# Optimization experiments

Measured on AMD Instinct MI355X. Metric: run time of the kernel, lower is better.

## Reference

```python
import jax, jax.numpy as jnp
import numpy as np

L, B, T, D, H, F, V = 4, 2, 1024, 1024, 16, 4096, 32000
DH = D // H
POWER = 4
EPS = 1e-6


def _anorm(x, gain):
    # y = g * x / (mean(|x|) + eps)  (L1 'diamond' norm)
    return gain * (x / (jnp.mean(jnp.abs(x), axis=-1, keepdims=True) + EPS))


def _rational_softmax(x):
    s = x / (jnp.abs(x) + 1.0)          # squash to (-1, 1)
    p = ((s + 1.0) * 0.5) ** POWER      # shift to (0,1), sharpen
    return p / (jnp.sum(p, axis=-1, keepdims=True) + EPS)


def setup_inputs() -> dict:
    key = jax.random.key(0)
    ks = jax.random.split(key, 12)
    w = 0.02  # weight scale for stability
    return {
        "idx": jax.random.randint(ks[0], (B, T), 0, V),
        "tok_emb": jax.random.normal(ks[1], (V, D), jnp.float32) * w,
        "pos_emb": jax.random.normal(ks[2], (T, D), jnp.float32) * w,
        "Wq": jax.random.normal(ks[3], (L, D, D), jnp.float32) * w,
        "bq": jnp.zeros((L, D), jnp.float32),
        "Wk": jax.random.normal(ks[4], (L, D, D), jnp.float32) * w,
        "bk": jnp.zeros((L, D), jnp.float32),
        "Wv": jax.random.normal(ks[5], (L, D, D), jnp.float32) * w,
        "bv": jnp.zeros((L, D), jnp.float32),
        "Wo": jax.random.normal(ks[6], (L, D, D), jnp.float32) * w,
        "bo": jnp.zeros((L, D), jnp.float32),
        "score_gain": jnp.full((L,), 4.0, jnp.float32),
        "norm1_gain": jnp.ones((L, D), jnp.float32),
        "norm2_gain": jnp.ones((L, D), jnp.float32),
        "W1": jax.random.normal(ks[7], (L, D, F), jnp.float32) * w,
        "b1": jnp.zeros((L, F), jnp.float32),
        "W2": jax.random.normal(ks[8], (L, F, D), jnp.float32) * w,
        "b2": jnp.zeros((L, D), jnp.float32),
        "final_gain": jnp.ones((D,), jnp.float32),
        "Wlm": jax.random.normal(ks[9], (D, V), jnp.float32) * w,
        "blm": jnp.zeros((V,), jnp.float32),
    }


def _forward(idx, tok_emb, pos_emb, Wq, bq, Wk, bk, Wv, bv, Wo, bo,
             score_gain, norm1_gain, norm2_gain, W1, b1, W2, b2,
             final_gain, Wlm, blm):
    Bx, Tx = idx.shape
    x = tok_emb[idx] + pos_emb[:Tx]                 # [B,T,D]
    mask = jnp.triu(jnp.ones((Tx, Tx), bool), 1)    # causal mask (True = masked)
    for l in range(L):
        # --- algebraic attention ---
        h = _anorm(x, norm1_gain[l])
        q = (h @ Wq[l] + bq[l]).reshape(Bx, Tx, H, DH).transpose(0, 2, 1, 3)
        k = (h @ Wk[l] + bk[l]).reshape(Bx, Tx, H, DH).transpose(0, 2, 1, 3)
        v = (h @ Wv[l] + bv[l]).reshape(Bx, Tx, H, DH).transpose(0, 2, 1, 3)
        scores = jnp.einsum('bhqd,bhkd->bhqk', q, k)
        scores = scores - jnp.mean(scores, axis=-1, keepdims=True)
        mad = jnp.mean(jnp.abs(scores), axis=-1, keepdims=True) + EPS
        scores = (scores / mad) * score_gain[l]
        scores = jnp.where(mask, -1000.0, scores)
        attn = _rational_softmax(scores)
        o = jnp.einsum('bhqk,bhkd->bhqd', attn, v)
        o = o.transpose(0, 2, 1, 3).reshape(Bx, Tx, D)
        x = x + (o @ Wo[l] + bo[l])
        # --- FFN with algebraic ReLU ---
        h = _anorm(x, norm2_gain[l])
        h = jnp.maximum(h @ W1[l] + b1[l], 0.0)
        x = x + (h @ W2[l] + b2[l])
    x = _anorm(x, final_gain)
    return x @ Wlm + blm                            # [B,T,V] logits


def reference(idx, tok_emb, pos_emb, Wq, bq, Wk, bk, Wv, bv, Wo, bo,
              score_gain, norm1_gain, norm2_gain, W1, b1, W2, b2,
              final_gain, Wlm, blm):
    return _forward(idx, tok_emb, pos_emb, Wq, bq, Wk, bk, Wv, bv, Wo, bo,
                    score_gain, norm1_gain, norm2_gain, W1, b1, W2, b2,
                    final_gain, Wlm, blm)
```

## Files before the change

### kernel.cpp

```cpp
#include <hip/hip_runtime.h>

typedef unsigned short u16;
typedef __bf16 bf16x8 __attribute__((ext_vector_type(8)));
typedef float f32x4 __attribute__((ext_vector_type(4)));
typedef unsigned int u32;

#define EPSF 1e-6f

__device__ __forceinline__ u16 f2bf(float f) {
  union { float f; unsigned u; } un; un.f = f;
  unsigned r = un.u + 0x7FFFu + ((un.u >> 16) & 1u);
  return (u16)(r >> 16);
}

__device__ __forceinline__ float block_sum(float v) {
  #pragma unroll
  for (int off = 32; off > 0; off >>= 1) v += __shfl_xor(v, off, 64);
  __shared__ float ws[4];
  const int w = threadIdx.x >> 6;
  __syncthreads();
  if ((threadIdx.x & 63) == 0) ws[w] = v;
  __syncthreads();
  return ws[0] + ws[1] + ws[2] + ws[3];
}

__device__ __forceinline__ void lds_cp16(const void* g, void* l) {
  __builtin_amdgcn_global_load_lds(
      (__attribute__((address_space(1))) void*)g,
      (__attribute__((address_space(3))) void*)l, 16, 0, 0);
}

__global__ __launch_bounds__(256) void embed_norm(
    const int* __restrict__ idx, const float* __restrict__ tok,
    const float* __restrict__ pos, const float* __restrict__ gain,
    float* __restrict__ x, u16* __restrict__ h) {
  const int row = blockIdx.x;
  const int tpos = row & 1023;
  const int token = idx[row];
  const int d = threadIdx.x * 4;
  const float4 a = *(const float4*)(tok + (long)token * 1024 + d);
  const float4 b = *(const float4*)(pos + (long)tpos * 1024 + d);
  float4 o; o.x = a.x + b.x; o.y = a.y + b.y; o.z = a.z + b.z; o.w = a.w + b.w;
  *(float4*)(x + (long)row * 1024 + d) = o;
  float s = fabsf(o.x) + fabsf(o.y) + fabsf(o.z) + fabsf(o.w);
  s = block_sum(s);
  const float scale = 1.0f / (s * (1.0f / 1024.0f) + EPSF);
  const float4 g = *(const float4*)(gain + d);
  ushort4 ov;
  ov.x = f2bf(o.x * g.x * scale);
  ov.y = f2bf(o.y * g.y * scale);
  ov.z = f2bf(o.z * g.z * scale);
  ov.w = f2bf(o.w * g.w * scale);
  *(ushort4*)(h + (long)row * 1024 + d) = ov;
}

__global__ __launch_bounds__(256) void anorm_kernel(
    const float* __restrict__ x, const float* __restrict__ gain,
    u16* __restrict__ h) {
  const int row = blockIdx.x;
  const int tid = threadIdx.x;
  const float4 v = *(const float4*)(x + (long)row * 1024 + tid * 4);
  float s = fabsf(v.x) + fabsf(v.y) + fabsf(v.z) + fabsf(v.w);
  s = block_sum(s);
  const float scale = 1.0f / (s * (1.0f / 1024.0f) + EPSF);
  const float4 g = *(const float4*)(gain + tid * 4);
  ushort4 o;
  o.x = f2bf(v.x * g.x * scale);
  o.y = f2bf(v.y * g.y * scale);
  o.z = f2bf(v.z * g.z * scale);
  o.w = f2bf(v.w * g.w * scale);
  *(ushort4*)(h + (long)row * 1024 + tid * 4) = o;
}

__global__ __launch_bounds__(512, 4) void attn_v4(
    const u16* __restrict__ qkv, const u16* __restrict__ v_t,
    u16* __restrict__ obuf, const float* __restrict__ score_gain, int l) {
  __shared__ float red1[2][4][16], red2[2][4][16], red3[2][4][16];
  __shared__ float Ured[2][4][16][68];
  __shared__ u16 Pl[8][640];
  const int qt = blockIdx.x, h = blockIdx.y, b = blockIdx.z;
  const int tid = threadIdx.x, w = tid >> 6, l64 = tid & 63;
  const int lq = l64 & 15, kgrp = l64 >> 4;
  const int wq = w >> 2, tq = w & 3;
  const int qglob = qt * 32 + wq * 16 + lq;
  const int qmax  = qt * 32 + wq * 16 + 15;
  const int tbase = tq * 256;
  const u16* Qg = qkv + (size_t)b * (1024 * 3072) + h * 64;
  const u16* Kg = Qg + 1024;
  const u16* Vt = v_t + (size_t)(b * 16 + h) * (64 * 1024);
  char* Pw = (char*)&Pl[w][0];

  bf16x8 qB0, qB1;
  {
    const u16* qp = Qg + (size_t)qglob * 3072 + (kgrp << 3);
    qB0 = *(const bf16x8*)qp;
    qB1 = *(const bf16x8*)(qp + 32);
  }

  f32x4 s[16];
  {
    const u16* Kl = Kg + (size_t)(tbase + lq) * 3072 + (kgrp << 3);
    #pragma unroll
    for (int tile = 0; tile < 16; tile++) {
      const u16* kp = Kl + (size_t)tile * (16 * 3072);
      const bf16x8 k0 = *(const bf16x8*)kp;
      const bf16x8 k1 = *(const bf16x8*)(kp + 32);
      f32x4 d = {0.f, 0.f, 0.f, 0.f};
      d = __builtin_amdgcn_mfma_f32_16x16x32_bf16(k0, qB0, d, 0, 0, 0);
      d = __builtin_amdgcn_mfma_f32_16x16x32_bf16(k1, qB1, d, 0, 0, 0);
      s[tile] = d;
    }
  }

  float ssum = 0.f;
  #pragma unroll
  for (int tile = 0; tile < 16; tile++)
    ssum += (s[tile][0] + s[tile][1]) + (s[tile][2] + s[tile][3]);
  ssum += __shfl_xor(ssum, 16, 64);
  ssum += __shfl_xor(ssum, 32, 64);
  if (l64 < 16) red1[wq][tq][l64] = ssum;
  __syncthreads();
  const float mean = (red1[wq][0][lq] + red1[wq][1][lq] +
                      red1[wq][2][lq] + red1[wq][3][lq]) * (1.0f / 1024.0f);

  float asum = 0.f;
  #pragma unroll
  for (int tile = 0; tile < 16; tile++)
    asum += fabsf(s[tile][0] - mean) + fabsf(s[tile][1] - mean) +
            fabsf(s[tile][2] - mean) + fabsf(s[tile][3] - mean);
  asum += __shfl_xor(asum, 16, 64);
  asum += __shfl_xor(asum, 32, 64);
  if (l64 < 16) red2[wq][tq][l64] = asum;
  __syncthreads();
  const float mad = (red2[wq][0][lq] + red2[wq][1][lq] +
                     red2[wq][2][lq] + red2[wq][3][lq]) * (1.0f / 1024.0f) + EPSF;
  const float gs = score_gain[l] / mad;

  float psum = 0.f;
  #pragma unroll
  for (int tile = 0; tile < 16; tile++) {
    #pragma unroll
    for (int j = 0; j < 4; j++) {
      const int t = tbase + tile * 16 + (kgrp << 2) + j;
      float sv = (s[tile][j] - mean) * gs;
      if (t > qglob) sv = -1000.0f;
      const float rr = sv / (fabsf(sv) + 1.0f);
      const float a1 = (rr + 1.0f) * 0.5f;
      const float a2 = a1 * a1;
      s[tile][j] = a2 * a2;
      psum += s[tile][j];
    }
  }

  f32x4 U[4] = {};
  #pragma unroll
  for (int c = 0; c < 8; c++) {
    const int t0 = tbase + c * 32;
    if (t0 <= qmax) {
      #pragma unroll
      for (int half = 0; half < 2; half++) {
        #pragma unroll
        for (int pr = 0; pr < 2; pr++) {
          const u32 pk = (u32)f2bf(s[2 * c + half][pr * 2]) |
                         ((u32)f2bf(s[2 * c + half][pr * 2 + 1]) << 16);
          *(u32*)(Pw + lq * 80 + half * 32 + (kgrp << 3) + (pr << 2)) = pk;
        }
      }
      asm volatile("s_waitcnt lgkmcnt(0)" ::: "memory");
      __builtin_amdgcn_sched_barrier(0);
      const bf16x8 pB = *(const bf16x8*)(Pw + lq * 80 + (kgrp << 4));
      #pragma unroll
      for (int dt = 0; dt < 4; dt++) {
        const bf16x8 vA = *(const bf16x8*)(Vt + (size_t)((dt << 4) + lq) * 1024 +
                                           t0 + (kgrp << 3));
        U[dt] = __builtin_amdgcn_mfma_f32_16x16x32_bf16(vA, pB, U[dt], 0, 0, 0);
      }
    }
  }

  psum += __shfl_xor(psum, 16, 64);
  psum += __shfl_xor(psum, 32, 64);
  if (l64 < 16) red3[wq][tq][l64] = psum;
  #pragma unroll
  for (int dt = 0; dt < 4; dt++)
    *(float4*)&Ured[wq][tq][lq][(dt << 4) + (kgrp << 2)] = *(const float4*)&U[dt];
  __syncthreads();

  {
    const int qq = tid >> 4, dhseg = (tid & 15) << 2;
    const int fwq = qq >> 4, flq = qq & 15;
    const float fps = red3[fwq][0][flq] + red3[fwq][1][flq] +
                      red3[fwq][2][flq] + red3[fwq][3][flq];
    const float oinv = 1.0f / (fps + EPSF);
    float4 u0 = *(const float4*)&Ured[fwq][0][flq][dhseg];
    const float4 u1 = *(const float4*)&Ured[fwq][1][flq][dhseg];
    const float4 u2 = *(const float4*)&Ured[fwq][2][flq][dhseg];
    const float4 u3 = *(const float4*)&Ured[fwq][3][flq][dhseg];
    u0.x = (u0.x + u1.x + u2.x + u3.x) * oinv;
    u0.y = (u0.y + u1.y + u2.y + u3.y) * oinv;
    u0.z = (u0.z + u1.z + u2.z + u3.z) * oinv;
    u0.w = (u0.w + u1.w + u2.w + u3.w) * oinv;
    ushort4 o;
    o.x = f2bf(u0.x); o.y = f2bf(u0.y); o.z = f2bf(u0.z); o.w = f2bf(u0.w);
    u16* dst = obuf + ((size_t)((b << 10) + qt * 32 + qq) << 10) + (h << 6) + dhseg;
    *(ushort4*)dst = o;
  }
}

__global__ void wconv_all(
    const float* __restrict__ Wq, const float* __restrict__ Wk,
    const float* __restrict__ Wv, const float* __restrict__ Wo,
    const float* __restrict__ W1, const float* __restrict__ W2,
    const float* __restrict__ Wlm,
    u16* __restrict__ wqkv_t, u16* __restrict__ wo_t,
    u16* __restrict__ w1_t, u16* __restrict__ w2_t, u16* __restrict__ wlm_t) {
  __shared__ float tile[64][65];
  const int bid = blockIdx.x;
  const float* src; u16* dst; int R, C, c0, r0;
  if (bid < 4096) {
    const int l = bid >> 10, m = (bid >> 8) & 3, t = bid & 255;
    if (m == 0)      src = Wq + (size_t)l * 1048576;
    else if (m == 1) src = Wk + (size_t)l * 1048576;
    else if (m == 2) src = Wv + (size_t)l * 1048576;
    else             src = Wo + (size_t)l * 1048576;
    dst = (m < 3) ? wqkv_t + ((size_t)l * 3072 + m * 1024) * 1024
                  : wo_t + (size_t)l * 1048576;
    R = 1024; C = 1024; c0 = (t & 15) << 6; r0 = (t >> 4) << 6;
  } else if (bid < 8192) {
    const int i = bid - 4096, l = i >> 10, t = i & 1023;
    src = W1 + (size_t)l * 4194304; dst = w1_t + (size_t)l * 4194304;
    R = 1024; C = 4096; c0 = (t & 63) << 6; r0 = (t >> 6) << 6;
  } else if (bid < 12288) {
    const int i = bid - 8192, l = i >> 10, t = i & 1023;
    src = W2 + (size_t)l * 4194304; dst = w2_t + (size_t)l * 4194304;
    R = 4096; C = 1024; c0 = (t & 15) << 6; r0 = (t >> 4) << 6;
  } else {
    const int i = bid - 12288;
    src = Wlm; dst = wlm_t;
    R = 1024; C = 32000; c0 = (i % 500) << 6; r0 = (i / 500) << 6;
  }
  const int tx = threadIdx.x, ty = threadIdx.y;
  const int cg = (tx & 15) << 2;
  const int rg = tx >> 4;
  #pragma unroll
  for (int i = 0; i < 4; i++) {
    const int row = i * 16 + ty * 4 + rg;
    const float4 v = *(const float4*)&src[(long)(r0 + row) * C + c0 + cg];
    tile[row][cg] = v.x; tile[row][cg + 1] = v.y;
    tile[row][cg + 2] = v.z; tile[row][cg + 3] = v.w;
  }
  __syncthreads();
  #pragma unroll
  for (int i = 0; i < 4; i++) {
    const int c = i * 16 + ty * 4 + rg;
    ushort4 o;
    o.x = f2bf(tile[cg][c]);     o.y = f2bf(tile[cg + 1][c]);
    o.z = f2bf(tile[cg + 2][c]); o.w = f2bf(tile[cg + 3][c]);
    *(ushort4*)&dst[(long)(c0 + c) * R + r0 + cg] = o;
  }
}

__global__ __launch_bounds__(256) void bias_concat(
    const float* __restrict__ bq, const float* __restrict__ bk,
    const float* __restrict__ bv, float* __restrict__ out) {
  const int i = blockIdx.x * 256 + threadIdx.x;
  const int l = i / 3072, j = i % 3072;
  float v;
  if (j < 1024)      v = bq[l * 1024 + j];
  else if (j < 2048) v = bk[l * 1024 + j - 1024];
  else               v = bv[l * 1024 + j - 2048];
  out[i] = v;
}

__global__ __launch_bounds__(256) void ffn2_reduce_norm(
    const float* __restrict__ part, const float* __restrict__ b2,
    float* __restrict__ x, const float* __restrict__ gain,
    u16* __restrict__ h) {
  const int row = blockIdx.x, c = threadIdx.x * 4;
  const float4 p0 = *(const float4*)(part + (size_t)row * 1024 + c);
  const float4 p1 = *(const float4*)(part + (size_t)(row + 2048) * 1024 + c);
  const float4 p2 = *(const float4*)(part + (size_t)(row + 4096) * 1024 + c);
  const float4 p3 = *(const float4*)(part + (size_t)(row + 6144) * 1024 + c);
  const float4 bb = *(const float4*)(b2 + c);
  float4 xv = *(float4*)(x + (size_t)row * 1024 + c);
  xv.x += (p0.x + p1.x) + (p2.x + p3.x) + bb.x;
  xv.y += (p0.y + p1.y) + (p2.y + p3.y) + bb.y;
  xv.z += (p0.z + p1.z) + (p2.z + p3.z) + bb.z;
  xv.w += (p0.w + p1.w) + (p2.w + p3.w) + bb.w;
  *(float4*)(x + (size_t)row * 1024 + c) = xv;
  float s = fabsf(xv.x) + fabsf(xv.y) + fabsf(xv.z) + fabsf(xv.w);
  s = block_sum(s);
  const float scale = 1.0f / (s * (1.0f / 1024.0f) + EPSF);
  const float4 g = *(const float4*)(gain + c);
  ushort4 o;
  o.x = f2bf(xv.x * g.x * scale);
  o.y = f2bf(xv.y * g.y * scale);
  o.z = f2bf(xv.z * g.z * scale);
  o.w = f2bf(xv.w * g.w * scale);
  *(ushort4*)(h + (size_t)row * 1024 + c) = o;
}

template <bool OUT_BF16, bool BIAS, bool RELU, bool RESID>
__global__ __launch_bounds__(512) void gemm256_kernel(
    const u16* __restrict__ A, long lda,
    const u16* __restrict__ Bt, long ldb,
    void* __restrict__ Cv, long ldc,
    const float* __restrict__ bias, const float* __restrict__ resid,
    int M, int N, int K, int nTM) {
  __shared__ u16 lds[65536];
  const int nwg = gridDim.x;
  const int qx = nwg >> 3, rx = nwg & 7;
  const int xcd = blockIdx.x & 7, seq = blockIdx.x >> 3;
  const int wg = (xcd < rx ? xcd * (qx + 1) : rx * (qx + 1) + (xcd - rx) * qx) + seq;
  const int tm = wg % nTM, tn = wg / nTM;
  const int rowA0 = tm * 256, rowB0 = tn * 256;

  const int t = threadIdx.x, w = t >> 6, l = t & 63;
  const int lrow = l & 15, kgrp = l >> 4;
  const int wr = w >> 2, wc = w & 3;

  const int srow = t >> 2;
  const int scol = ((t & 3) ^ ((t >> 3) & 3)) * 8;
  const u16* Asrc = A + (long)(rowA0 + srow) * lda + scol;
  const u16* Bsrc = Bt + (long)(rowB0 + srow) * ldb + scol;
  char* ldsB = (char*)lds;
  const int wbase = w * 1024;

  const int fswz = (kgrp ^ ((lrow >> 1) & 3)) * 8;
  const int aoff = (wr * 128 + lrow) * 32 + fswz;
  const int boff = 8192 + (wc * 64 + lrow) * 32 + fswz;

  f32x4 acc[8][4] = {};
  const int NT = K >> 5;

  #pragma unroll
  for (int pt = 0; pt < 3; pt++) {
    const int k0 = pt << 5;
    const int bb = pt * 32768;
    lds_cp16(Asrc + k0,                    ldsB + bb + wbase);
    lds_cp16(Asrc + (long)128 * lda + k0,  ldsB + bb + 8192 + wbase);
    lds_cp16(Bsrc + k0,                    ldsB + bb + 16384 + wbase);
    lds_cp16(Bsrc + (long)128 * ldb + k0,  ldsB + bb + 24576 + wbase);
  }

  for (int tt = 0; tt < NT; tt++) {
    const int rem = NT - 1 - tt;
    if (rem >= 2)      asm volatile("s_waitcnt vmcnt(8)" ::: "memory");
    else if (rem == 1) asm volatile("s_waitcnt vmcnt(4)" ::: "memory");
    else               asm volatile("s_waitcnt vmcnt(0)" ::: "memory");
    __builtin_amdgcn_sched_barrier(0);
    __builtin_amdgcn_s_barrier();

    const u16* buf = lds + (tt & 3) * 16384;
    const int stage = tt + 3 < NT;
    const int k0n = (tt + 3) << 5;
    const int bbn = ((tt + 3) & 3) * 32768;

    bf16x8 aF[4], bF[4];
    #pragma unroll
    for (int m = 0; m < 4; m++) aF[m] = *(const bf16x8*)(buf + aoff + m * 512);
    #pragma unroll
    for (int n = 0; n < 4; n++) bF[n] = *(const bf16x8*)(buf + boff + n * 512);
    if (stage) {
      lds_cp16(Asrc + k0n,                   ldsB + bbn + wbase);
      lds_cp16(Asrc + (long)128 * lda + k0n, ldsB + bbn + 8192 + wbase);
    }
    asm volatile("s_waitcnt lgkmcnt(0)" ::: "memory");
    __builtin_amdgcn_sched_barrier(0);
    __builtin_amdgcn_s_setprio(1);
    #pragma unroll
    for (int m = 0; m < 4; m++)
      #pragma unroll
      for (int n = 0; n < 4; n++)
        acc[m][n] = __builtin_amdgcn_mfma_f32_16x16x32_bf16(aF[m], bF[n], acc[m][n], 0, 0, 0);
    __builtin_amdgcn_s_setprio(0);

    #pragma unroll
    for (int m = 0; m < 4; m++) aF[m] = *(const bf16x8*)(buf + aoff + (m + 4) * 512);
    if (stage) {
      lds_cp16(Bsrc + k0n,                   ldsB + bbn + 16384 + wbase);
      lds_cp16(Bsrc + (long)128 * ldb + k0n, ldsB + bbn + 24576 + wbase);
    }
    asm volatile("s_waitcnt lgkmcnt(0)" ::: "memory");
    __builtin_amdgcn_sched_barrier(0);
    __builtin_amdgcn_s_setprio(1);
    #pragma unroll
    for (int m = 0; m < 4; m++)
      #pragma unroll
      for (int n = 0; n < 4; n++)
        acc[m + 4][n] = __builtin_amdgcn_mfma_f32_16x16x32_bf16(aF[m], bF[n], acc[m + 4][n], 0, 0, 0);
    __builtin_amdgcn_s_setprio(0);
  }

  float bvv[4];
  #pragma unroll
  for (int n = 0; n < 4; n++)
    bvv[n] = BIAS ? bias[rowB0 + wc * 64 + n * 16 + lrow] : 0.0f;
  #pragma unroll
  for (int m = 0; m < 8; m++) {
    const int row = rowA0 + wr * 128 + m * 16 + kgrp * 4;
    #pragma unroll
    for (int n = 0; n < 4; n++) {
      const int col = rowB0 + wc * 64 + n * 16 + lrow;
      #pragma unroll
      for (int j = 0; j < 4; j++) {
        float v = acc[m][n][j] + bvv[n];
        if (RELU) v = fmaxf(v, 0.0f);
        const long off = (long)(row + j) * ldc + col;
        if (RESID) v += resid[off];
        if (OUT_BF16) ((u16*)Cv)[off] = f2bf(v);
        else          ((float*)Cv)[off] = v;
      }
    }
  }
}

template <bool OUT_BF16, bool BIAS, bool RELU, bool RESID, bool VTOUT>
__global__ __launch_bounds__(256) void gemm128p(
    const u16* __restrict__ A, long lda, long sA,
    const u16* __restrict__ Bt, long ldb, long sB,
    void* __restrict__ Cv, long ldc, long sC,
    const float* __restrict__ bias, const float* __restrict__ resid,
    u16* __restrict__ vtout,
    int M, int N, int K, int nTM) {
  __shared__ u16 lds[32768];
  const int nwg = gridDim.x;
  const int qx = nwg >> 3, rx = nwg & 7;
  const int xcd = blockIdx.x & 7, seq = blockIdx.x >> 3;
  const int wg = (xcd < rx ? xcd * (qx + 1) : rx * (qx + 1) + (xcd - rx) * qx) + seq;
  const int tm = wg % nTM, tn = wg / nTM;
  const int batch = blockIdx.y;
  A  += (long)batch * sA;
  Bt += (long)batch * sB;
  const int rowA0 = tm * 128, rowB0 = tn * 128;
  const int t = threadIdx.x, w = t >> 6, l = t & 63;
  const int lrow = l & 15, kgrp = l >> 4;
  const int wr = (w >> 1) << 6, wc = (w & 1) << 6;

  const int srow = t >> 2;
  const int scol = ((t & 3) ^ ((t >> 3) & 3)) * 8;
  const u16* Asrc = A + (long)(rowA0 + srow) * lda + scol;
  const u16* Bsrc = Bt + (long)(rowB0 + srow) * ldb + scol;
  char* ldsB = (char*)lds;
  const int wbase = w * 1024;

  const int swz8 = (kgrp ^ ((lrow >> 1) & 3)) * 8;
  const int aoff = (wr + lrow) * 32 + swz8;
  const int boff = 4096 + (wc + lrow) * 32 + swz8;

  f32x4 acc[4][4] = {};
  const int NT = K >> 5;

  #pragma unroll
  for (int pt = 0; pt < 3; pt++) {
    const int k0 = pt << 5;
    const int bb = pt * 16384;
    lds_cp16(Asrc + k0,                   ldsB + bb + wbase);
    lds_cp16(Asrc + (long)64 * lda + k0,  ldsB + bb + 4096 + wbase);
    lds_cp16(Bsrc + k0,                   ldsB + bb + 8192 + wbase);
    lds_cp16(Bsrc + (long)64 * ldb + k0,  ldsB + bb + 12288 + wbase);
  }

  for (int tt = 0; tt < NT; tt++) {
    const int rem = NT - 1 - tt;
    if (rem >= 2)      asm volatile("s_waitcnt vmcnt(8)" ::: "memory");
    else if (rem == 1) asm volatile("s_waitcnt vmcnt(4)" ::: "memory");
    else               asm volatile("s_waitcnt vmcnt(0)" ::: "memory");
    __builtin_amdgcn_sched_barrier(0);
    __builtin_amdgcn_s_barrier();

    const u16* buf = lds + (tt & 3) * 8192;
    const int stage = tt + 3 < NT;
    const int k0n = (tt + 3) << 5;
    const int bbn = ((tt + 3) & 3) * 16384;

    bf16x8 aF[4], bF[4];
    #pragma unroll
    for (int m = 0; m < 4; m++) aF[m] = *(const bf16x8*)(buf + aoff + m * 512);
    #pragma unroll
    for (int n = 0; n < 4; n++) bF[n] = *(const bf16x8*)(buf + boff + n * 512);
    if (stage) {
      lds_cp16(Asrc + k0n,                  ldsB + bbn + wbase);
      lds_cp16(Asrc + (long)64 * lda + k0n, ldsB + bbn + 4096 + wbase);
      lds_cp16(Bsrc + k0n,                  ldsB + bbn + 8192 + wbase);
      lds_cp16(Bsrc + (long)64 * ldb + k0n, ldsB + bbn + 12288 + wbase);
    }
    asm volatile("s_waitcnt lgkmcnt(0)" ::: "memory");
    __builtin_amdgcn_sched_barrier(0);
    __builtin_amdgcn_s_setprio(1);
    #pragma unroll
    for (int m = 0; m < 4; m++)
      #pragma unroll
      for (int n = 0; n < 4; n++)
        acc[m][n] = __builtin_amdgcn_mfma_f32_16x16x32_bf16(aF[m], bF[n], acc[m][n], 0, 0, 0);
    __builtin_amdgcn_s_setprio(0);
  }

  if (VTOUT && rowB0 >= 2048) {
    __syncthreads();
    #pragma unroll
    for (int m = 0; m < 4; m++) {
      #pragma unroll
      for (int n = 0; n < 4; n++) {
        const int c = wc + n * 16 + lrow;
        const int r = wr + m * 16 + (kgrp << 2);
        ushort4 pk;
        float v0 = acc[m][n][0], v1 = acc[m][n][1], v2 = acc[m][n][2], v3 = acc[m][n][3];
        if (BIAS) {
          const float bv = bias[rowB0 + c];
          v0 += bv; v1 += bv; v2 += bv; v3 += bv;
        }
        pk.x = f2bf(v0); pk.y = f2bf(v1); pk.z = f2bf(v2); pk.w = f2bf(v3);
        *(ushort4*)&lds[c * 136 + r] = pk;
      }
    }
    __syncthreads();
    {
      const int c = t >> 1, half = t & 1;
      const int dh = c & 63;
      const int h = ((rowB0 - 2048) >> 6) + (c >> 6);
      const int bb2 = rowA0 >> 10, t0 = rowA0 & 1023;
      u16* dst = vtout + (((size_t)(bb2 * 16 + h)) << 16) + ((size_t)dh << 10) +
                 t0 + half * 64;
      #pragma unroll
      for (int k = 0; k < 8; k++)
        *(bf16x8*)(dst + k * 8) = *(const bf16x8*)&lds[c * 136 + half * 64 + k * 8];
    }
  } else {
    const long coff = (long)batch * sC;
    #pragma unroll
    for (int m = 0; m < 4; m++) {
      #pragma unroll
      for (int n = 0; n < 4; n++) {
        const int col = rowB0 + wc + n * 16 + lrow;
        #pragma unroll
        for (int j = 0; j < 4; j++) {
          const int row = rowA0 + wr + m * 16 + (kgrp << 2) + j;
          float v = acc[m][n][j];
          if (BIAS) v += bias[col];
          if (RELU) v = fmaxf(v, 0.0f);
          const long off = coff + (long)row * ldc + col;
          if (RESID) v += resid[off];
          if (OUT_BF16) ((u16*)Cv)[off] = f2bf(v);
          else          ((float*)Cv)[off] = v;
        }
      }
    }
  }
}

extern "C" void kernel_launch(void* const* d_in, const int* in_sizes, int n_in,
                              void* d_out, int out_size, void* d_ws, size_t ws_size,
                              hipStream_t stream) {
  constexpr int Lc = 4, Tc = 1024, Dc = 1024, Hc = 16, Fc = 4096, DHc = 64;
  const int M = 2 * Tc;

  const int*   idxp       = (const int*)  d_in[0];
  const float* tok_emb    = (const float*)d_in[1];
  const float* pos_emb    = (const float*)d_in[2];
  const float* Wq         = (const float*)d_in[3];
  const float* bq         = (const float*)d_in[4];
  const float* Wk         = (const float*)d_in[5];
  const float* bk         = (const float*)d_in[6];
  const float* Wv         = (const float*)d_in[7];
  const float* bv         = (const float*)d_in[8];
  const float* Wo         = (const float*)d_in[9];
  const float* bo         = (const float*)d_in[10];
  const float* score_gain = (const float*)d_in[11];
  const float* norm1_gain = (const float*)d_in[12];
  const float* norm2_gain = (const float*)d_in[13];
  const float* W1         = (const float*)d_in[14];
  const float* b1         = (const float*)d_in[15];
  const float* W2         = (const float*)d_in[16];
  const float* b2         = (const float*)d_in[17];
  const float* final_gain = (const float*)d_in[18];
  const float* Wlm        = (const float*)d_in[19];
  const float* blm        = (const float*)d_in[20];

  char* p = (char*)d_ws;
  auto alloc = [&](size_t n) { char* r = p; p += (n + 255) & ~(size_t)255; return r; };
  u16*  wqkv_t = (u16*) alloc((size_t)Lc * 3072 * 1024 * 2);
  u16*  wo_t   = (u16*) alloc((size_t)Lc * 1024 * 1024 * 2);
  u16*  w1_t   = (u16*) alloc((size_t)Lc * 4096 * 1024 * 2);
  u16*  w2_t   = (u16*) alloc((size_t)Lc * 1024 * 4096 * 2);
  u16*  wlm_t  = (u16*) alloc((size_t)32000 * 1024 * 2);
  float* bqkv  = (float*)alloc((size_t)Lc * 3072 * 4);
  float* x     = (float*)alloc((size_t)M * 1024 * 4);
  u16*  hbuf   = (u16*) alloc((size_t)M * 1024 * 2);
  u16*  qkv    = (u16*) alloc((size_t)M * 3072 * 2);
  u16*  v_t    = (u16*) alloc((size_t)2 * Hc * DHc * Tc * 2);
  u16*  obuf   = (u16*) alloc((size_t)M * 1024 * 2);
  u16*  ffh    = (u16*) alloc((size_t)M * 4096 * 2);
  float* fpart = (float*)alloc((size_t)4 * M * 1024 * 4);

  wconv_all<<<20288, dim3(64, 4), 0, stream>>>(Wq, Wk, Wv, Wo, W1, W2, Wlm,
                                               wqkv_t, wo_t, w1_t, w2_t, wlm_t);
  bias_concat<<<48, 256, 0, stream>>>(bq, bk, bv, bqkv);
  embed_norm<<<M, 256, 0, stream>>>(idxp, tok_emb, pos_emb, norm1_gain, x, hbuf);

  for (int l = 0; l < Lc; l++) {
    gemm128p<true, true, false, false, true><<<dim3(16 * 24, 1), 256, 0, stream>>>(
        hbuf, 1024, 0, wqkv_t + (size_t)l * 3072 * 1024, 1024, 0,
        qkv, 3072, 0, bqkv + (size_t)l * 3072, nullptr, v_t, M, 3072, 1024, 16);

    attn_v4<<<dim3(32, 16, 2), 512, 0, stream>>>(qkv, v_t, obuf, score_gain, l);

    gemm128p<false, true, false, true, false><<<dim3(16 * 8, 1), 256, 0, stream>>>(
        obuf, 1024, 0, wo_t + (size_t)l * 1024 * 1024, 1024, 0,
        x, 1024, 0, bo + (size_t)l * 1024, x, nullptr, M, 1024, 1024, 16);
    anorm_kernel<<<M, 256, 0, stream>>>(x, norm2_gain + (size_t)l * Dc, hbuf);
    gemm128p<true, true, true, false, false><<<dim3(16 * 32, 1), 256, 0, stream>>>(
        hbuf, 1024, 0, w1_t + (size_t)l * Fc * Dc, 1024, 0,
        ffh, 4096, 0, b1 + (size_t)l * Fc, nullptr, nullptr, M, 4096, 1024, 16);
    gemm128p<false, false, false, false, false><<<dim3(128, 4), 256, 0, stream>>>(
        ffh, 4096, 1024, w2_t + (size_t)l * Dc * Fc, 4096, 1024,
        fpart, 1024, (long)M * 1024, nullptr, nullptr, nullptr, M, 1024, 1024, 16);
    const float* gnext = (l < Lc - 1) ? (norm1_gain + (size_t)(l + 1) * Dc) : final_gain;
    ffn2_reduce_norm<<<M, 256, 0, stream>>>(fpart, b2 + (size_t)l * Dc, x, gnext, hbuf);
  }

  gemm256_kernel<false, true, false, false><<<dim3(1000), 512, 0, stream>>>(
      hbuf, 1024, wlm_t, 1024,
      d_out, 32000, blm, nullptr, M, 32000, 1024, 8);
}
```

Before: 990.9 us.

## Interleave attention key tiles across waves and split-K the output projection

```diff
diff --git a/kernel.cpp b/kernel.cpp
--- a/kernel.cpp
+++ b/kernel.cpp
@@ -54,25 +54,7 @@
   *(ushort4*)(h + (long)row * 1024 + d) = ov;
 }
 
-__global__ __launch_bounds__(256) void anorm_kernel(
-    const float* __restrict__ x, const float* __restrict__ gain,
-    u16* __restrict__ h) {
-  const int row = blockIdx.x;
-  const int tid = threadIdx.x;
-  const float4 v = *(const float4*)(x + (long)row * 1024 + tid * 4);
-  float s = fabsf(v.x) + fabsf(v.y) + fabsf(v.z) + fabsf(v.w);
-  s = block_sum(s);
-  const float scale = 1.0f / (s * (1.0f / 1024.0f) + EPSF);
-  const float4 g = *(const float4*)(gain + tid * 4);
-  ushort4 o;
-  o.x = f2bf(v.x * g.x * scale);
-  o.y = f2bf(v.y * g.y * scale);
-  o.z = f2bf(v.z * g.z * scale);
-  o.w = f2bf(v.w * g.w * scale);
-  *(ushort4*)(h + (long)row * 1024 + tid * 4) = o;
-}
-
-__global__ __launch_bounds__(512, 4) void attn_v4(
+__global__ __launch_bounds__(512, 4) void attn_v5(
     const u16* __restrict__ qkv, const u16* __restrict__ v_t,
     u16* __restrict__ obuf, const float* __restrict__ score_gain, int l) {
   __shared__ float red1[2][4][16], red2[2][4][16], red3[2][4][16];
@@ -84,7 +66,6 @@
   const int wq = w >> 2, tq = w & 3;
   const int qglob = qt * 32 + wq * 16 + lq;
   const int qmax  = qt * 32 + wq * 16 + 15;
-  const int tbase = tq * 256;
   const u16* Qg = qkv + (size_t)b * (1024 * 3072) + h * 64;
   const u16* Kg = Qg + 1024;
   const u16* Vt = v_t + (size_t)(b * 16 + h) * (64 * 1024);
@@ -99,23 +80,24 @@
 
   f32x4 s[16];
   {
-    const u16* Kl = Kg + (size_t)(tbase + lq) * 3072 + (kgrp << 3);
-    #pragma unroll
-    for (int tile = 0; tile < 16; tile++) {
-      const u16* kp = Kl + (size_t)tile * (16 * 3072);
+    const u16* Ktq = Kg + (size_t)(tq * 32 + lq) * 3072 + (kgrp << 3);
+    #pragma unroll
+    for (int tl = 0; tl < 16; tl++) {
+      const int cst = ((tl >> 1) << 7) + ((tl & 1) << 4);
+      const u16* kp = Ktq + (size_t)cst * 3072;
       const bf16x8 k0 = *(const bf16x8*)kp;
       const bf16x8 k1 = *(const bf16x8*)(kp + 32);
       f32x4 d = {0.f, 0.f, 0.f, 0.f};
       d = __builtin_amdgcn_mfma_f32_16x16x32_bf16(k0, qB0, d, 0, 0, 0);
       d = __builtin_amdgcn_mfma_f32_16x16x32_bf16(k1, qB1, d, 0, 0, 0);
-      s[tile] = d;
+      s[tl] = d;
     }
   }
 
   float ssum = 0.f;
   #pragma unroll
-  for (int tile = 0; tile < 16; tile++)
-    ssum += (s[tile][0] + s[tile][1]) + (s[tile][2] + s[tile][3]);
+  for (int tl = 0; tl < 16; tl++)
+    ssum += (s[tl][0] + s[tl][1]) + (s[tl][2] + s[tl][3]);
   ssum += __shfl_xor(ssum, 16, 64);
   ssum += __shfl_xor(ssum, 32, 64);
   if (l64 < 16) red1[wq][tq][l64] = ssum;
@@ -125,9 +107,9 @@
 
   float asum = 0.f;
   #pragma unroll
-  for (int tile = 0; tile < 16; tile++)
-    asum += fabsf(s[tile][0] - mean) + fabsf(s[tile][1] - mean) +
-            fabsf(s[tile][2] - mean) + fabsf(s[tile][3] - mean);
+  for (int tl = 0; tl < 16; tl++)
+    asum += fabsf(s[tl][0] - mean) + fabsf(s[tl][1] - mean) +
+            fabsf(s[tl][2] - mean) + fabsf(s[tl][3] - mean);
   asum += __shfl_xor(asum, 16, 64);
   asum += __shfl_xor(asum, 32, 64);
   if (l64 < 16) red2[wq][tq][l64] = asum;
@@ -138,42 +120,47 @@
 
   float psum = 0.f;
   #pragma unroll
-  for (int tile = 0; tile < 16; tile++) {
+  for (int tl = 0; tl < 16; tl++) {
+    const int tbase = tq * 32 + ((tl >> 1) << 7) + ((tl & 1) << 4);
     #pragma unroll
     for (int j = 0; j < 4; j++) {
-      const int t = tbase + tile * 16 + (kgrp << 2) + j;
-      float sv = (s[tile][j] - mean) * gs;
+      const int t = tbase + (kgrp << 2) + j;
+      float sv = (s[tl][j] - mean) * gs;
       if (t > qglob) sv = -1000.0f;
       const float rr = sv / (fabsf(sv) + 1.0f);
       const float a1 = (rr + 1.0f) * 0.5f;
       const float a2 = a1 * a1;
-      s[tile][j] = a2 * a2;
-      psum += s[tile][j];
+      s[tl][j] = a2 * a2;
+      psum += s[tl][j];
     }
   }
 
   f32x4 U[4] = {};
-  #pragma unroll
-  for (int c = 0; c < 8; c++) {
-    const int t0 = tbase + c * 32;
-    if (t0 <= qmax) {
-      #pragma unroll
-      for (int half = 0; half < 2; half++) {
+  {
+    const u16* Vtq = Vt + (size_t)lq * 1024 + tq * 32 + (kgrp << 3);
+    #pragma unroll
+    for (int cc = 0; cc < 8; cc++) {
+      const int t0 = tq * 32 + (cc << 7);
+      if (t0 <= qmax) {
+        bf16x8 vA[4];
         #pragma unroll
-        for (int pr = 0; pr < 2; pr++) {
-          const u32 pk = (u32)f2bf(s[2 * c + half][pr * 2]) |
-                         ((u32)f2bf(s[2 * c + half][pr * 2 + 1]) << 16);
-          *(u32*)(Pw + lq * 80 + half * 32 + (kgrp << 3) + (pr << 2)) = pk;
+        for (int dt = 0; dt < 4; dt++)
+          vA[dt] = *(const bf16x8*)(Vtq + (size_t)(dt << 4) * 1024 + (cc << 7));
+        #pragma unroll
+        for (int half = 0; half < 2; half++) {
+          #pragma unroll
+          for (int pr = 0; pr < 2; pr++) {
+            const u32 pk = (u32)f2bf(s[2 * cc + half][pr * 2]) |
+                           ((u32)f2bf(s[2 * cc + half][pr * 2 + 1]) << 16);
+            *(u32*)(Pw + lq * 80 + half * 32 + (kgrp << 3) + (pr << 2)) = pk;
+          }
         }
-      }
-      asm volatile("s_waitcnt lgkmcnt(0)" ::: "memory");
-      __builtin_amdgcn_sched_barrier(0);
-      const bf16x8 pB = *(const bf16x8*)(Pw + lq * 80 + (kgrp << 4));
-      #pragma unroll
-      for (int dt = 0; dt < 4; dt++) {
-        const bf16x8 vA = *(const bf16x8*)(Vt + (size_t)((dt << 4) + lq) * 1024 +
-                                           t0 + (kgrp << 3));
-        U[dt] = __builtin_amdgcn_mfma_f32_16x16x32_bf16(vA, pB, U[dt], 0, 0, 0);
+        asm volatile("s_waitcnt lgkmcnt(0)" ::: "memory");
+        __builtin_amdgcn_sched_barrier(0);
+        const bf16x8 pB = *(const bf16x8*)(Pw + lq * 80 + (kgrp << 4));
+        #pragma unroll
+        for (int dt = 0; dt < 4; dt++)
+          U[dt] = __builtin_amdgcn_mfma_f32_16x16x32_bf16(vA[dt], pB, U[dt], 0, 0, 0);
       }
     }
   }
@@ -272,21 +259,24 @@
   out[i] = v;
 }
 
-__global__ __launch_bounds__(256) void ffn2_reduce_norm(
-    const float* __restrict__ part, const float* __restrict__ b2,
+template <int NPART>
+__global__ __launch_bounds__(256) void reduce_norm(
+    const float* __restrict__ part, const float* __restrict__ bias,
     float* __restrict__ x, const float* __restrict__ gain,
     u16* __restrict__ h) {
   const int row = blockIdx.x, c = threadIdx.x * 4;
-  const float4 p0 = *(const float4*)(part + (size_t)row * 1024 + c);
-  const float4 p1 = *(const float4*)(part + (size_t)(row + 2048) * 1024 + c);
-  const float4 p2 = *(const float4*)(part + (size_t)(row + 4096) * 1024 + c);
-  const float4 p3 = *(const float4*)(part + (size_t)(row + 6144) * 1024 + c);
-  const float4 bb = *(const float4*)(b2 + c);
+  float4 acc = *(const float4*)(part + (size_t)row * 1024 + c);
+  #pragma unroll
+  for (int i = 1; i < NPART; i++) {
+    const float4 pi = *(const float4*)(part + (size_t)(row + i * 2048) * 1024 + c);
+    acc.x += pi.x; acc.y += pi.y; acc.z += pi.z; acc.w += pi.w;
+  }
+  const float4 bb = *(const float4*)(bias + c);
   float4 xv = *(float4*)(x + (size_t)row * 1024 + c);
-  xv.x += (p0.x + p1.x) + (p2.x + p3.x) + bb.x;
-  xv.y += (p0.y + p1.y) + (p2.y + p3.y) + bb.y;
-  xv.z += (p0.z + p1.z) + (p2.z + p3.z) + bb.z;
-  xv.w += (p0.w + p1.w) + (p2.w + p3.w) + bb.w;
+  xv.x += acc.x + bb.x;
+  xv.y += acc.y + bb.y;
+  xv.z += acc.z + bb.z;
+  xv.w += acc.w + bb.w;
   *(float4*)(x + (size_t)row * 1024 + c) = xv;
   float s = fabsf(xv.x) + fabsf(xv.y) + fabsf(xv.z) + fabsf(xv.w);
   s = block_sum(s);
@@ -603,12 +593,13 @@
         hbuf, 1024, 0, wqkv_t + (size_t)l * 3072 * 1024, 1024, 0,
         qkv, 3072, 0, bqkv + (size_t)l * 3072, nullptr, v_t, M, 3072, 1024, 16);
 
-    attn_v4<<<dim3(32, 16, 2), 512, 0, stream>>>(qkv, v_t, obuf, score_gain, l);
-
-    gemm128p<false, true, false, true, false><<<dim3(16 * 8, 1), 256, 0, stream>>>(
-        obuf, 1024, 0, wo_t + (size_t)l * 1024 * 1024, 1024, 0,
-        x, 1024, 0, bo + (size_t)l * 1024, x, nullptr, M, 1024, 1024, 16);
-    anorm_kernel<<<M, 256, 0, stream>>>(x, norm2_gain + (size_t)l * Dc, hbuf);
+    attn_v5<<<dim3(32, 16, 2), 512, 0, stream>>>(qkv, v_t, obuf, score_gain, l);
+
+    gemm128p<false, false, false, false, false><<<dim3(128, 2), 256, 0, stream>>>(
+        obuf, 1024, 512, wo_t + (size_t)l * 1024 * 1024, 1024, 512,
+        fpart, 1024, (long)M * 1024, nullptr, nullptr, nullptr, M, 1024, 512, 16);
+    reduce_norm<2><<<M, 256, 0, stream>>>(fpart, bo + (size_t)l * Dc, x,
+                                          norm2_gain + (size_t)l * Dc, hbuf);
     gemm128p<true, true, true, false, false><<<dim3(16 * 32, 1), 256, 0, stream>>>(
         hbuf, 1024, 0, w1_t + (size_t)l * Fc * Dc, 1024, 0,
         ffh, 4096, 0, b1 + (size_t)l * Fc, nullptr, nullptr, M, 4096, 1024, 16);
@@ -616,7 +607,7 @@
         ffh, 4096, 1024, w2_t + (size_t)l * Dc * Fc, 4096, 1024,
         fpart, 1024, (long)M * 1024, nullptr, nullptr, nullptr, M, 1024, 1024, 16);
     const float* gnext = (l < Lc - 1) ? (norm1_gain + (size_t)(l + 1) * Dc) : final_gain;
-    ffn2_reduce_norm<<<M, 256, 0, stream>>>(fpart, b2 + (size_t)l * Dc, x, gnext, hbuf);
+    reduce_norm<4><<<M, 256, 0, stream>>>(fpart, b2 + (size_t)l * Dc, x, gnext, hbuf);
   }
 
   gemm256_kernel<false, true, false, false><<<dim3(1000), 512, 0, stream>>>(
```

After: 978.9 us, median of 3. No clear change (-1.2%).
